# Kernel tuning notes

Hardware: AMD Instinct MI355X
Metric: run time of the kernel (lower is better)

## Reference

```python
import jax, jax.numpy as jnp
import numpy as np

B, T, D, H = 2, 2048, 1024, 16
DH = D // H  # head_dim = 64
ROPE_BASE = 10000.0


def _rope_cos_sin(seq_len, dh, dtype):
    inv_freq = 1.0 / (ROPE_BASE ** (jnp.arange(0, dh, 2, dtype=jnp.float32) / dh))
    t = jnp.arange(seq_len, dtype=jnp.float32)
    freqs = jnp.outer(t, inv_freq)            # [T, dh/2]
    emb = jnp.concatenate([freqs, freqs], -1)  # [T, dh]
    return jnp.cos(emb).astype(dtype), jnp.sin(emb).astype(dtype)


def _rotate_half(x):
    half = x.shape[-1] // 2
    return jnp.concatenate([-x[..., half:], x[..., :half]], axis=-1)


def setup_inputs() -> dict:
    key = jax.random.key(0)
    k1, k2, k3 = jax.random.split(key, 3)
    x = jax.random.normal(k1, (B, T, D), dtype=jnp.float32)
    w_qkv = jax.random.normal(k2, (D, 3 * D), dtype=jnp.float32) * (D ** -0.5)
    w_out = jax.random.normal(k3, (D, D), dtype=jnp.float32) * (D ** -0.5)
    return {"x": x, "w_qkv": w_qkv, "w_out": w_out}


def reference(x, w_qkv, w_out):
    b, t, _ = x.shape
    qkv = x @ w_qkv                                        # [B,T,3D]
    qkv = qkv.reshape(b, t, 3, H, DH).transpose(2, 0, 3, 1, 4)  # [3,B,H,T,DH]
    q, k, v = qkv[0], qkv[1], qkv[2]

    cos, sin = _rope_cos_sin(t, DH, x.dtype)               # [T,DH] each
    q = q * cos + _rotate_half(q) * sin
    k = k * cos + _rotate_half(k) * sin

    scale = DH ** -0.5
    scores = jnp.einsum('bhtd,bhsd->bhts', q, k) * scale   # [B,H,T,T]
    # dense additive causal mask (as in original module)
    neg = jnp.finfo(x.dtype).min
    causal = jnp.triu(jnp.ones((t, t), dtype=bool), k=1)
    scores = scores + jnp.where(causal, neg, jnp.zeros((), x.dtype))
    attn = jax.nn.softmax(scores, axis=-1)
    out = jnp.einsum('bhts,bhsd->bhtd', attn, v)           # [B,H,T,DH]
    out = out.transpose(0, 2, 1, 3).reshape(b, t, D)       # [B,T,D]
    return out @ w_out
```

## Files before the change

### kernel.cpp

```cpp
#include <hip/hip_runtime.h>

typedef __bf16 bf16x8 __attribute__((ext_vector_type(8)));
typedef float f32x4 __attribute__((ext_vector_type(4)));
typedef unsigned int u32x4 __attribute__((ext_vector_type(4)));
typedef unsigned int u32x2 __attribute__((ext_vector_type(2)));
typedef unsigned short u16;
typedef unsigned int u32;

#define BSZ 2
#define TSEQ 2048
#define DMODEL 1024
#define NHEAD 16
#define DHEAD 64

#define GLDS(gp, lp)                                                        \
  __builtin_amdgcn_global_load_lds(                                         \
      (const __attribute__((address_space(1))) void*)(gp),                  \
      (__attribute__((address_space(3))) void*)(lp), 16, 0, 0)

#define TRR(dst, base, OFF)                                                 \
  asm volatile("ds_read_b64_tr_b16 %0, %1 offset:" OFF                     \
               : "=v"(dst) : "v"(base) : "memory")

__device__ __forceinline__ u16 f2bf(float f) {
  return __builtin_bit_cast(u16, (__bf16)f);
}
__device__ __forceinline__ float bf2f(u16 h) {
  return __builtin_bit_cast(float, (u32)h << 16);
}

__global__ void k_cvt(const float* __restrict__ in, u16* __restrict__ out, int n4) {
  int i = blockIdx.x * 256 + threadIdx.x;
  if (i >= n4) return;
  float4 v = ((const float4*)in)[i];
  ushort4 o;
  o.x = f2bf(v.x); o.y = f2bf(v.y); o.z = f2bf(v.z); o.w = f2bf(v.w);
  ((ushort4*)out)[i] = o;
}

__global__ void k_transpose_cvt(const float* __restrict__ in, u16* __restrict__ out,
                                int K, int N) {
  __shared__ float tile[64][65];
  int n0 = blockIdx.x * 64, k0 = blockIdx.y * 64;
  int tx = threadIdx.x & 63, ty = threadIdx.x >> 6;
#pragma unroll
  for (int i = ty; i < 64; i += 4)
    tile[i][tx] = in[(size_t)(k0 + i) * N + n0 + tx];
  __syncthreads();
#pragma unroll
  for (int i = ty; i < 64; i += 4)
    out[(size_t)(n0 + i) * K + k0 + tx] = f2bf(tile[tx][i]);
}

__global__ void k_rope_table(float* __restrict__ cosT, float* __restrict__ sinT) {
  int idx = blockIdx.x * 256 + threadIdx.x;
  int t = idx >> 5, f = idx & 31;
  float inv_freq = powf(10000.0f, -(float)(2 * f) / 64.0f);
  float ang = (float)t * inv_freq;
  float s, c;
  sincosf(ang, &s, &c);
  cosT[idx] = c;
  sinT[idx] = s;
}

template <typename OutT>
__global__ __launch_bounds__(256) void k_gemm(const u16* __restrict__ A,
                                              const u16* __restrict__ Bt,
                                              OutT* __restrict__ C, int M, int N, int K) {
  __shared__ __align__(16) u16 a_lds[2][128][32];
  __shared__ __align__(16) u16 b_lds[2][128][32];
  int m0 = blockIdx.y * 128, n0 = blockIdx.x * 128;
  int tid = threadIdx.x;
  int w = tid >> 6, l = tid & 63, lr = l & 15, lg = l >> 4;
  int wr = (w >> 1) * 64, wc = (w & 1) * 64;
  int grow = l >> 2;
  int gcol = (l & 3) * 8;
  f32x4 acc[4][4] = {};

  const u16* a0 = A + (size_t)(m0 + w * 16 + grow) * K + gcol;
  const u16* a1 = A + (size_t)(m0 + (w + 4) * 16 + grow) * K + gcol;
  const u16* b0 = Bt + (size_t)(n0 + w * 16 + grow) * K + gcol;
  const u16* b1 = Bt + (size_t)(n0 + (w + 4) * 16 + grow) * K + gcol;

  int NT = K >> 5;
  GLDS(a0, &a_lds[0][w * 16][0]);
  GLDS(a1, &a_lds[0][(w + 4) * 16][0]);
  GLDS(b0, &b_lds[0][w * 16][0]);
  GLDS(b1, &b_lds[0][(w + 4) * 16][0]);

  for (int t = 0; t < NT; ++t) {
    int p = t & 1;
    if (t + 1 < NT) {
      int k0 = (t + 1) << 5;
      GLDS(a0 + k0, &a_lds[p ^ 1][w * 16][0]);
      GLDS(a1 + k0, &a_lds[p ^ 1][(w + 4) * 16][0]);
      GLDS(b0 + k0, &b_lds[p ^ 1][w * 16][0]);
      GLDS(b1 + k0, &b_lds[p ^ 1][(w + 4) * 16][0]);
      asm volatile("s_waitcnt vmcnt(4)" ::: "memory");
    } else {
      asm volatile("s_waitcnt vmcnt(0)" ::: "memory");
    }
    __builtin_amdgcn_s_barrier();
    __builtin_amdgcn_sched_barrier(0);
    bf16x8 af[4], bfv[4];
#pragma unroll
    for (int mt = 0; mt < 4; ++mt)
      af[mt] = __builtin_bit_cast(bf16x8, *(const u32x4*)&a_lds[p][wr + mt * 16 + lr][lg * 8]);
#pragma unroll
    for (int nt = 0; nt < 4; ++nt)
      bfv[nt] = __builtin_bit_cast(bf16x8, *(const u32x4*)&b_lds[p][wc + nt * 16 + lr][lg * 8]);
    __builtin_amdgcn_s_setprio(1);
#pragma unroll
    for (int mt = 0; mt < 4; ++mt)
#pragma unroll
      for (int nt = 0; nt < 4; ++nt)
        acc[mt][nt] = __builtin_amdgcn_mfma_f32_16x16x32_bf16(af[mt], bfv[nt], acc[mt][nt], 0, 0, 0);
    __builtin_amdgcn_s_setprio(0);
    __builtin_amdgcn_sched_barrier(0);
    __builtin_amdgcn_s_barrier();
  }

#pragma unroll
  for (int mt = 0; mt < 4; ++mt)
#pragma unroll
    for (int nt = 0; nt < 4; ++nt)
#pragma unroll
      for (int r = 0; r < 4; ++r) {
        int row = m0 + wr + mt * 16 + lg * 4 + r;
        int col = n0 + wc + nt * 16 + lr;
        C[(size_t)row * N + col] = acc[mt][nt][r];
      }
}

__global__ __launch_bounds__(256) void k_gemm_qkv(const u16* __restrict__ A,
                                                  const u16* __restrict__ Bt,
                                                  u16* __restrict__ Qh, u16* __restrict__ Kh,
                                                  u16* __restrict__ Vh,
                                                  const float* __restrict__ cosT,
                                                  const float* __restrict__ sinT) {
  const int M = BSZ * TSEQ, N = 3 * DMODEL, K = DMODEL;
  __shared__ __align__(16) u16 a_lds[2][128][32];
  __shared__ __align__(16) u16 b_lds[2][128][32];
  int m0 = blockIdx.y * 128, n0 = blockIdx.x * 128;
  int tid = threadIdx.x;
  int w = tid >> 6, l = tid & 63, lr = l & 15, lg = l >> 4;
  int wr = (w >> 1) * 64, wc = (w & 1) * 64;
  int grow = l >> 2;
  int gcol = (l & 3) * 8;
  f32x4 acc[4][4] = {};

  const u16* a0 = A + (size_t)(m0 + w * 16 + grow) * K + gcol;
  const u16* a1 = A + (size_t)(m0 + (w + 4) * 16 + grow) * K + gcol;
  const u16* b0 = Bt + (size_t)(n0 + w * 16 + grow) * K + gcol;
  const u16* b1 = Bt + (size_t)(n0 + (w + 4) * 16 + grow) * K + gcol;

  int NT = K >> 5;
  GLDS(a0, &a_lds[0][w * 16][0]);
  GLDS(a1, &a_lds[0][(w + 4) * 16][0]);
  GLDS(b0, &b_lds[0][w * 16][0]);
  GLDS(b1, &b_lds[0][(w + 4) * 16][0]);

  for (int t = 0; t < NT; ++t) {
    int p = t & 1;
    if (t + 1 < NT) {
      int k0 = (t + 1) << 5;
      GLDS(a0 + k0, &a_lds[p ^ 1][w * 16][0]);
      GLDS(a1 + k0, &a_lds[p ^ 1][(w + 4) * 16][0]);
      GLDS(b0 + k0, &b_lds[p ^ 1][w * 16][0]);
      GLDS(b1 + k0, &b_lds[p ^ 1][(w + 4) * 16][0]);
      asm volatile("s_waitcnt vmcnt(4)" ::: "memory");
    } else {
      asm volatile("s_waitcnt vmcnt(0)" ::: "memory");
    }
    __builtin_amdgcn_s_barrier();
    __builtin_amdgcn_sched_barrier(0);
    bf16x8 af[4], bfv[4];
#pragma unroll
    for (int mt = 0; mt < 4; ++mt)
      af[mt] = __builtin_bit_cast(bf16x8, *(const u32x4*)&a_lds[p][wr + mt * 16 + lr][lg * 8]);
#pragma unroll
    for (int nt = 0; nt < 4; ++nt)
      bfv[nt] = __builtin_bit_cast(bf16x8, *(const u32x4*)&b_lds[p][wc + nt * 16 + lr][lg * 8]);
    __builtin_amdgcn_s_setprio(1);
#pragma unroll
    for (int mt = 0; mt < 4; ++mt)
#pragma unroll
      for (int nt = 0; nt < 4; ++nt)
        acc[mt][nt] = __builtin_amdgcn_mfma_f32_16x16x32_bf16(af[mt], bfv[nt], acc[mt][nt], 0, 0, 0);
    __builtin_amdgcn_s_setprio(0);
    __builtin_amdgcn_sched_barrier(0);
    __builtin_amdgcn_s_barrier();
  }

  int sec = n0 >> 10;
  int hcol = ((n0 + wc) & 1023) >> 6;
  u16* outp = (sec == 0) ? Qh : (sec == 1) ? Kh : Vh;
  float qscale = (sec == 0) ? 0.125f : 1.0f;
#pragma unroll
  for (int mt = 0; mt < 4; ++mt)
#pragma unroll
    for (int r = 0; r < 4; ++r) {
      int row = m0 + wr + mt * 16 + lg * 4 + r;
      int b = row >> 11, tt = row & 2047;
      size_t obase = ((size_t)((b * 16 + hcol) * 2048 + tt)) * 64;
      if (sec == 2) {
#pragma unroll
        for (int nt = 0; nt < 4; ++nt)
          outp[obase + nt * 16 + lr] = f2bf(acc[mt][nt][r]);
      } else {
        float c0 = cosT[tt * 32 + lr],      s0 = sinT[tt * 32 + lr];
        float c1 = cosT[tt * 32 + 16 + lr], s1 = sinT[tt * 32 + 16 + lr];
        float v0 = acc[mt][0][r], v1 = acc[mt][1][r];
        float v2 = acc[mt][2][r], v3 = acc[mt][3][r];
        outp[obase + lr]      = f2bf((v0 * c0 - v2 * s0) * qscale);
        outp[obase + 16 + lr] = f2bf((v1 * c1 - v3 * s1) * qscale);
        outp[obase + 32 + lr] = f2bf((v2 * c0 + v0 * s0) * qscale);
        outp[obase + 48 + lr] = f2bf((v3 * c1 + v1 * s1) * qscale);
      }
    }
}

__global__ __launch_bounds__(256) void k_flash(const u16* __restrict__ Qg, const u16* __restrict__ Kg,
                                               const u16* __restrict__ Vg, u16* __restrict__ O) {
  __shared__ __align__(16) u16 k_lds[2][64][72];
  __shared__ __align__(16) u16 vsub[2][4096];
  __shared__ __align__(16) u16 p_lds[4][16][68];
  int pairIdx = blockIdx.x;
  int bh = blockIdx.y;
  int b = bh >> 4, h = bh & 15;
  size_t hoff = (size_t)bh * TSEQ * DHEAD;
  int tid = threadIdx.x, w = tid >> 6, l = tid & 63, lr = l & 15, lg = l >> 4;

  int srow = tid >> 3;
  int g8 = tid & 7;
  int sc8 = g8 * 8;
  u32 vtr0 = (u32)(uintptr_t)vsub + (u32)(lg * 1024 + lr * 8);

  const u16* kbase = Kg + hoff;
  const u16* vbase = Vg + hoff;

  for (int sub = 0; sub < 2; ++sub) {
    int qb = sub == 0 ? (31 - pairIdx) : pairIdx;

    int qrow = qb * 64 + w * 16 + lr;
    const u16* qp = Qg + hoff + (size_t)qrow * 64 + lg * 8;
    bf16x8 qf0 = __builtin_bit_cast(bf16x8, *(const u32x4*)qp);
    bf16x8 qf1 = __builtin_bit_cast(bf16x8, *(const u32x4*)(qp + 32));

    f32x4 acc[4] = {};
    float mrow[4] = {-1e30f, -1e30f, -1e30f, -1e30f};
    float lrow[4] = {0.f, 0.f, 0.f, 0.f};

    u32x4 kreg[2], vreg[2];
#pragma unroll
    for (int p = 0; p < 2; ++p) {
      int r = srow + p * 32;
      kreg[p] = *(const u32x4*)(kbase + (size_t)r * 64 + sc8);
      vreg[p] = *(const u32x4*)(vbase + (size_t)r * 64 + sc8);
    }
    __syncthreads();

    for (int kv = 0; kv <= qb; ++kv) {
      int cur = kv & 1;
#pragma unroll
      for (int p = 0; p < 2; ++p) {
        int r = srow + p * 32;
        *(u32x4*)&k_lds[cur][r][sc8] = kreg[p];
        int vo = ((r >> 2) * 4 + (g8 >> 1)) * 64 + (r & 3) * 16 + (g8 & 1) * 8;
        *(u32x4*)&vsub[cur][vo] = vreg[p];
      }
      __syncthreads();
      if (kv < qb) {
#pragma unroll
        for (int p = 0; p < 2; ++p) {
          int r = (kv + 1) * 64 + srow + p * 32;
          kreg[p] = *(const u32x4*)(kbase + (size_t)r * 64 + sc8);
          vreg[p] = *(const u32x4*)(vbase + (size_t)r * 64 + sc8);
        }
      }

      f32x4 s[4];
      __builtin_amdgcn_s_setprio(1);
#pragma unroll
      for (int c = 0; c < 4; ++c) {
        const u16* kp2 = &k_lds[cur][c * 16 + lr][lg * 8];
        bf16x8 kf0 = __builtin_bit_cast(bf16x8, *(const u32x4*)kp2);
        bf16x8 kf1 = __builtin_bit_cast(bf16x8, *(const u32x4*)(kp2 + 32));
        f32x4 z = {};
        z = __builtin_amdgcn_mfma_f32_16x16x32_bf16(qf0, kf0, z, 0, 0, 0);
        s[c] = __builtin_amdgcn_mfma_f32_16x16x32_bf16(qf1, kf1, z, 0, 0, 0);
      }
      __builtin_amdgcn_s_setprio(0);
      if (kv == qb) {
#pragma unroll
        for (int c = 0; c < 4; ++c)
#pragma unroll
          for (int r = 0; r < 4; ++r)
            if (c * 16 + lr > w * 16 + lg * 4 + r) s[c][r] = -1e30f;
      }

      float rmax[4];
#pragma unroll
      for (int r = 0; r < 4; ++r)
        rmax[r] = fmaxf(fmaxf(s[0][r], s[1][r]), fmaxf(s[2][r], s[3][r]));
#pragma unroll
      for (int mset = 1; mset <= 8; mset <<= 1)
#pragma unroll
        for (int r = 0; r < 4; ++r)
          rmax[r] = fmaxf(rmax[r], __shfl_xor(rmax[r], mset, 64));
      bool need = (rmax[0] > mrow[0] + 8.0f) | (rmax[1] > mrow[1] + 8.0f) |
                  (rmax[2] > mrow[2] + 8.0f) | (rmax[3] > mrow[3] + 8.0f);
      if (__any(need)) {
        float alpha[4];
#pragma unroll
        for (int r = 0; r < 4; ++r) {
          float mn = fmaxf(mrow[r], rmax[r]);
          alpha[r] = __expf(mrow[r] - mn);
          mrow[r] = mn;
          lrow[r] *= alpha[r];
        }
#pragma unroll
        for (int n = 0; n < 4; ++n)
#pragma unroll
          for (int r = 0; r < 4; ++r)
            acc[n][r] *= alpha[r];
      }
#pragma unroll
      for (int c = 0; c < 4; ++c)
#pragma unroll
        for (int r = 0; r < 4; ++r) {
          float pe = __expf(s[c][r] - mrow[r]);
          s[c][r] = pe;
          lrow[r] += pe;
        }

#pragma unroll
      for (int c = 0; c < 4; ++c)
#pragma unroll
        for (int r = 0; r < 4; ++r)
          p_lds[w][lg * 4 + r][c * 16 + lr] = f2bf(s[c][r]);
      bf16x8 pa0 = __builtin_bit_cast(bf16x8, *(const u32x4*)&p_lds[w][lr][lg * 8]);
      bf16x8 pa1 = __builtin_bit_cast(bf16x8, *(const u32x4*)&p_lds[w][lr][lg * 8 + 32]);

      u32 vtr = vtr0 + (u32)(cur * 8192);
      {
        u32x2 t[8];
        TRR(t[0], vtr, "0");    TRR(t[1], vtr, "512");
        TRR(t[2], vtr, "4096"); TRR(t[3], vtr, "4608");
        TRR(t[4], vtr, "128");  TRR(t[5], vtr, "640");
        TRR(t[6], vtr, "4224"); TRR(t[7], vtr, "4736");
        asm volatile("s_waitcnt lgkmcnt(0)" ::: "memory");
        __builtin_amdgcn_sched_barrier(0);
        __builtin_amdgcn_s_setprio(1);
#pragma unroll
        for (int n2 = 0; n2 < 2; ++n2) {
          u32x4 vlo, vhi;
          vlo[0] = t[n2 * 4 + 0][0]; vlo[1] = t[n2 * 4 + 0][1];
          vlo[2] = t[n2 * 4 + 1][0]; vlo[3] = t[n2 * 4 + 1][1];
          vhi[0] = t[n2 * 4 + 2][0]; vhi[1] = t[n2 * 4 + 2][1];
          vhi[2] = t[n2 * 4 + 3][0]; vhi[3] = t[n2 * 4 + 3][1];
          acc[n2] = __builtin_amdgcn_mfma_f32_16x16x32_bf16(pa0, __builtin_bit_cast(bf16x8, vlo), acc[n2], 0, 0, 0);
          acc[n2] = __builtin_amdgcn_mfma_f32_16x16x32_bf16(pa1, __builtin_bit_cast(bf16x8, vhi), acc[n2], 0, 0, 0);
        }
        __builtin_amdgcn_s_setprio(0);
      }
      {
        u32x2 t[8];
        TRR(t[0], vtr, "256");  TRR(t[1], vtr, "768");
        TRR(t[2], vtr, "4352"); TRR(t[3], vtr, "4864");
        TRR(t[4], vtr, "384");  TRR(t[5], vtr, "896");
        TRR(t[6], vtr, "4480"); TRR(t[7], vtr, "4992");
        asm volatile("s_waitcnt lgkmcnt(0)" ::: "memory");
        __builtin_amdgcn_sched_barrier(0);
        __builtin_amdgcn_s_setprio(1);
#pragma unroll
        for (int n2 = 0; n2 < 2; ++n2) {
          int n = 2 + n2;
          u32x4 vlo, vhi;
          vlo[0] = t[n2 * 4 + 0][0]; vlo[1] = t[n2 * 4 + 0][1];
          vlo[2] = t[n2 * 4 + 1][0]; vlo[3] = t[n2 * 4 + 1][1];
          vhi[0] = t[n2 * 4 + 2][0]; vhi[1] = t[n2 * 4 + 2][1];
          vhi[2] = t[n2 * 4 + 3][0]; vhi[3] = t[n2 * 4 + 3][1];
          acc[n] = __builtin_amdgcn_mfma_f32_16x16x32_bf16(pa0, __builtin_bit_cast(bf16x8, vlo), acc[n], 0, 0, 0);
          acc[n] = __builtin_amdgcn_mfma_f32_16x16x32_bf16(pa1, __builtin_bit_cast(bf16x8, vhi), acc[n], 0, 0, 0);
        }
        __builtin_amdgcn_s_setprio(0);
      }
    }

#pragma unroll
    for (int mset = 1; mset <= 8; mset <<= 1)
#pragma unroll
      for (int r = 0; r < 4; ++r)
        lrow[r] += __shfl_xor(lrow[r], mset, 64);
#pragma unroll
    for (int n = 0; n < 4; ++n)
#pragma unroll
      for (int r = 0; r < 4; ++r) {
        int t = qb * 64 + w * 16 + lg * 4 + r;
        int dd = n * 16 + lr;
        float ov = acc[n][r] / lrow[r];
        O[(size_t)(b * TSEQ + t) * DMODEL + h * 64 + dd] = f2bf(ov);
      }
  }
}

extern "C" void kernel_launch(void* const* d_in, const int* in_sizes, int n_in,
                              void* d_out, int out_size, void* d_ws, size_t ws_size,
                              hipStream_t stream) {
  const float* x     = (const float*)d_in[0];
  const float* w_qkv = (const float*)d_in[1];
  const float* w_out = (const float*)d_in[2];
  float* out = (float*)d_out;

  char* ws = (char*)d_ws;
  size_t off = 0;
  auto alloc = [&](size_t bytes) {
    char* p = ws + off;
    off += (bytes + 255) & ~(size_t)255;
    return p;
  };
  const size_t MT = (size_t)BSZ * TSEQ;
  u16* xb    = (u16*)alloc(MT * DMODEL * 2);
  u16* wqkvT = (u16*)alloc((size_t)3 * DMODEL * DMODEL * 2);
  u16* woutT = (u16*)alloc((size_t)DMODEL * DMODEL * 2);
  u16* Qh    = (u16*)alloc(MT * DMODEL * 2);
  u16* Kh    = (u16*)alloc(MT * DMODEL * 2);
  u16* Vh    = (u16*)alloc(MT * DMODEL * 2);
  u16* aout  = (u16*)alloc(MT * DMODEL * 2);
  float* cosT = (float*)alloc((size_t)TSEQ * 32 * 4);
  float* sinT = (float*)alloc((size_t)TSEQ * 32 * 4);
  if (ws_size < off) return;

  k_cvt<<<(MT * DMODEL / 4 + 255) / 256, 256, 0, stream>>>(x, xb, MT * DMODEL / 4);
  k_transpose_cvt<<<dim3(48, 16), 256, 0, stream>>>(w_qkv, wqkvT, DMODEL, 3 * DMODEL);
  k_transpose_cvt<<<dim3(16, 16), 256, 0, stream>>>(w_out, woutT, DMODEL, DMODEL);
  k_rope_table<<<(TSEQ * 32) / 256, 256, 0, stream>>>(cosT, sinT);
  k_gemm_qkv<<<dim3(24, 32), 256, 0, stream>>>(xb, wqkvT, Qh, Kh, Vh, cosT, sinT);
  k_flash<<<dim3(16, BSZ * NHEAD), 256, 0, stream>>>(Qh, Kh, Vh, aout);
  k_gemm<float><<<dim3(8, 32), 256, 0, stream>>>(aout, woutT, out, (int)MT, DMODEL, DMODEL);
}
```

Before: 218.2 us.

## Fuse prep kernels, share K/V tiles across paired query blocks, shrink out-proj tile

```diff
diff --git a/kernel.cpp b/kernel.cpp
--- a/kernel.cpp
+++ b/kernel.cpp
@@ -25,48 +25,68 @@
 __device__ __forceinline__ u16 f2bf(float f) {
   return __builtin_bit_cast(u16, (__bf16)f);
 }
+__device__ __forceinline__ u32 pack2bf(float lo, float hi) {
+  return (u32)f2bf(lo) | ((u32)f2bf(hi) << 16);
+}
 __device__ __forceinline__ float bf2f(u16 h) {
   return __builtin_bit_cast(float, (u32)h << 16);
 }
 
-__global__ void k_cvt(const float* __restrict__ in, u16* __restrict__ out, int n4) {
-  int i = blockIdx.x * 256 + threadIdx.x;
-  if (i >= n4) return;
-  float4 v = ((const float4*)in)[i];
-  ushort4 o;
-  o.x = f2bf(v.x); o.y = f2bf(v.y); o.z = f2bf(v.z); o.w = f2bf(v.w);
-  ((ushort4*)out)[i] = o;
-}
-
-__global__ void k_transpose_cvt(const float* __restrict__ in, u16* __restrict__ out,
-                                int K, int N) {
+__global__ void k_prep(const float* __restrict__ x, u16* __restrict__ xb,
+                       const float* __restrict__ wqkv, u16* __restrict__ wqkvT,
+                       const float* __restrict__ wout, u16* __restrict__ woutT,
+                       float* __restrict__ cosT, float* __restrict__ sinT) {
   __shared__ float tile[64][65];
-  int n0 = blockIdx.x * 64, k0 = blockIdx.y * 64;
-  int tx = threadIdx.x & 63, ty = threadIdx.x >> 6;
-#pragma unroll
-  for (int i = ty; i < 64; i += 4)
-    tile[i][tx] = in[(size_t)(k0 + i) * N + n0 + tx];
-  __syncthreads();
-#pragma unroll
-  for (int i = ty; i < 64; i += 4)
-    out[(size_t)(n0 + i) * K + k0 + tx] = f2bf(tile[tx][i]);
-}
-
-__global__ void k_rope_table(float* __restrict__ cosT, float* __restrict__ sinT) {
-  int idx = blockIdx.x * 256 + threadIdx.x;
-  int t = idx >> 5, f = idx & 31;
-  float inv_freq = powf(10000.0f, -(float)(2 * f) / 64.0f);
-  float ang = (float)t * inv_freq;
-  float s, c;
-  sincosf(ang, &s, &c);
-  cosT[idx] = c;
-  sinT[idx] = s;
-}
-
-template <typename OutT>
-__global__ __launch_bounds__(256) void k_gemm(const u16* __restrict__ A,
-                                              const u16* __restrict__ Bt,
-                                              OutT* __restrict__ C, int M, int N, int K) {
+  int blk = blockIdx.x, tid = threadIdx.x;
+  if (blk < 2048) {
+    int i = blk * 256 + tid;
+    const float4* f4 = (const float4*)x;
+    float4 v0 = f4[i * 2], v1 = f4[i * 2 + 1];
+    u32x4 o;
+    o[0] = pack2bf(v0.x, v0.y); o[1] = pack2bf(v0.z, v0.w);
+    o[2] = pack2bf(v1.x, v1.y); o[3] = pack2bf(v1.z, v1.w);
+    ((u32x4*)xb)[i] = o;
+  } else if (blk < 2816) {
+    int idx = blk - 2048;
+    int n0 = (idx % 48) * 64, k0 = (idx / 48) * 64;
+    int tx = tid & 63, ty = tid >> 6;
+#pragma unroll
+    for (int i = ty; i < 64; i += 4)
+      tile[i][tx] = wqkv[(size_t)(k0 + i) * 3072 + n0 + tx];
+    __syncthreads();
+#pragma unroll
+    for (int i = ty; i < 64; i += 4)
+      wqkvT[(size_t)(n0 + i) * 1024 + k0 + tx] = f2bf(tile[tx][i]);
+  } else if (blk < 3072) {
+    int idx = blk - 2816;
+    int n0 = (idx % 16) * 64, k0 = (idx / 16) * 64;
+    int tx = tid & 63, ty = tid >> 6;
+#pragma unroll
+    for (int i = ty; i < 64; i += 4)
+      tile[i][tx] = wout[(size_t)(k0 + i) * 1024 + n0 + tx];
+    __syncthreads();
+#pragma unroll
+    for (int i = ty; i < 64; i += 4)
+      woutT[(size_t)(n0 + i) * 1024 + k0 + tx] = f2bf(tile[tx][i]);
+  } else {
+    int idx = (blk - 3072) * 256 + tid;
+    int t = idx >> 5, f = idx & 31;
+    float inv_freq = powf(10000.0f, -(float)(2 * f) / 64.0f);
+    float ang = (float)t * inv_freq;
+    float s, c;
+    sincosf(ang, &s, &c);
+    cosT[idx] = c;
+    sinT[idx] = s;
+  }
+}
+
+__global__ __launch_bounds__(256) void k_gemm_qkv(const u16* __restrict__ A,
+                                                  const u16* __restrict__ Bt,
+                                                  u16* __restrict__ Qh, u16* __restrict__ Kh,
+                                                  u16* __restrict__ Vh,
+                                                  const float* __restrict__ cosT,
+                                                  const float* __restrict__ sinT) {
+  const int K = DMODEL;
   __shared__ __align__(16) u16 a_lds[2][128][32];
   __shared__ __align__(16) u16 b_lds[2][128][32];
   int m0 = blockIdx.y * 128, n0 = blockIdx.x * 128;
@@ -120,78 +140,6 @@
     __builtin_amdgcn_s_barrier();
   }
 
-#pragma unroll
-  for (int mt = 0; mt < 4; ++mt)
-#pragma unroll
-    for (int nt = 0; nt < 4; ++nt)
-#pragma unroll
-      for (int r = 0; r < 4; ++r) {
-        int row = m0 + wr + mt * 16 + lg * 4 + r;
-        int col = n0 + wc + nt * 16 + lr;
-        C[(size_t)row * N + col] = acc[mt][nt][r];
-      }
-}
-
-__global__ __launch_bounds__(256) void k_gemm_qkv(const u16* __restrict__ A,
-                                                  const u16* __restrict__ Bt,
-                                                  u16* __restrict__ Qh, u16* __restrict__ Kh,
-                                                  u16* __restrict__ Vh,
-                                                  const float* __restrict__ cosT,
-                                                  const float* __restrict__ sinT) {
-  const int M = BSZ * TSEQ, N = 3 * DMODEL, K = DMODEL;
-  __shared__ __align__(16) u16 a_lds[2][128][32];
-  __shared__ __align__(16) u16 b_lds[2][128][32];
-  int m0 = blockIdx.y * 128, n0 = blockIdx.x * 128;
-  int tid = threadIdx.x;
-  int w = tid >> 6, l = tid & 63, lr = l & 15, lg = l >> 4;
-  int wr = (w >> 1) * 64, wc = (w & 1) * 64;
-  int grow = l >> 2;
-  int gcol = (l & 3) * 8;
-  f32x4 acc[4][4] = {};
-
-  const u16* a0 = A + (size_t)(m0 + w * 16 + grow) * K + gcol;
-  const u16* a1 = A + (size_t)(m0 + (w + 4) * 16 + grow) * K + gcol;
-  const u16* b0 = Bt + (size_t)(n0 + w * 16 + grow) * K + gcol;
-  const u16* b1 = Bt + (size_t)(n0 + (w + 4) * 16 + grow) * K + gcol;
-
-  int NT = K >> 5;
-  GLDS(a0, &a_lds[0][w * 16][0]);
-  GLDS(a1, &a_lds[0][(w + 4) * 16][0]);
-  GLDS(b0, &b_lds[0][w * 16][0]);
-  GLDS(b1, &b_lds[0][(w + 4) * 16][0]);
-
-  for (int t = 0; t < NT; ++t) {
-    int p = t & 1;
-    if (t + 1 < NT) {
-      int k0 = (t + 1) << 5;
-      GLDS(a0 + k0, &a_lds[p ^ 1][w * 16][0]);
-      GLDS(a1 + k0, &a_lds[p ^ 1][(w + 4) * 16][0]);
-      GLDS(b0 + k0, &b_lds[p ^ 1][w * 16][0]);
-      GLDS(b1 + k0, &b_lds[p ^ 1][(w + 4) * 16][0]);
-      asm volatile("s_waitcnt vmcnt(4)" ::: "memory");
-    } else {
-      asm volatile("s_waitcnt vmcnt(0)" ::: "memory");
-    }
-    __builtin_amdgcn_s_barrier();
-    __builtin_amdgcn_sched_barrier(0);
-    bf16x8 af[4], bfv[4];
-#pragma unroll
-    for (int mt = 0; mt < 4; ++mt)
-      af[mt] = __builtin_bit_cast(bf16x8, *(const u32x4*)&a_lds[p][wr + mt * 16 + lr][lg * 8]);
-#pragma unroll
-    for (int nt = 0; nt < 4; ++nt)
-      bfv[nt] = __builtin_bit_cast(bf16x8, *(const u32x4*)&b_lds[p][wc + nt * 16 + lr][lg * 8]);
-    __builtin_amdgcn_s_setprio(1);
-#pragma unroll
-    for (int mt = 0; mt < 4; ++mt)
-#pragma unroll
-      for (int nt = 0; nt < 4; ++nt)
-        acc[mt][nt] = __builtin_amdgcn_mfma_f32_16x16x32_bf16(af[mt], bfv[nt], acc[mt][nt], 0, 0, 0);
-    __builtin_amdgcn_s_setprio(0);
-    __builtin_amdgcn_sched_barrier(0);
-    __builtin_amdgcn_s_barrier();
-  }
-
   int sec = n0 >> 10;
   int hcol = ((n0 + wc) & 1023) >> 6;
   u16* outp = (sec == 0) ? Qh : (sec == 1) ? Kh : Vh;
@@ -220,12 +168,79 @@
     }
 }
 
+__global__ __launch_bounds__(256) void k_gemm_out(const u16* __restrict__ A,
+                                                  const u16* __restrict__ Bt,
+                                                  float* __restrict__ C) {
+  const int N = 1024, K = 1024;
+  __shared__ __align__(16) u16 a_lds[2][128][32];
+  __shared__ __align__(16) u16 b_lds[2][64][32];
+  int m0 = blockIdx.y * 128, n0 = blockIdx.x * 64;
+  int tid = threadIdx.x;
+  int w = tid >> 6, l = tid & 63, lr = l & 15, lg = l >> 4;
+  int wr = (w >> 1) * 64, wc = (w & 1) * 32;
+  int grow = l >> 2;
+  int gcol = (l & 3) * 8;
+  f32x4 acc[4][2] = {};
+
+  const u16* a0 = A + (size_t)(m0 + w * 16 + grow) * K + gcol;
+  const u16* a1 = A + (size_t)(m0 + (w + 4) * 16 + grow) * K + gcol;
+  const u16* b0 = Bt + (size_t)(n0 + w * 16 + grow) * K + gcol;
+
+  int NT = K >> 5;
+  GLDS(a0, &a_lds[0][w * 16][0]);
+  GLDS(a1, &a_lds[0][(w + 4) * 16][0]);
+  GLDS(b0, &b_lds[0][w * 16][0]);
+
+  for (int t = 0; t < NT; ++t) {
+    int p = t & 1;
+    if (t + 1 < NT) {
+      int k0 = (t + 1) << 5;
+      GLDS(a0 + k0, &a_lds[p ^ 1][w * 16][0]);
+      GLDS(a1 + k0, &a_lds[p ^ 1][(w + 4) * 16][0]);
+      GLDS(b0 + k0, &b_lds[p ^ 1][w * 16][0]);
+      asm volatile("s_waitcnt vmcnt(3)" ::: "memory");
+    } else {
+      asm volatile("s_waitcnt vmcnt(0)" ::: "memory");
+    }
+    __builtin_amdgcn_s_barrier();
+    __builtin_amdgcn_sched_barrier(0);
+    bf16x8 af[4], bfv[2];
+#pragma unroll
+    for (int mt = 0; mt < 4; ++mt)
+      af[mt] = __builtin_bit_cast(bf16x8, *(const u32x4*)&a_lds[p][wr + mt * 16 + lr][lg * 8]);
+#pragma unroll
+    for (int nt = 0; nt < 2; ++nt)
+      bfv[nt] = __builtin_bit_cast(bf16x8, *(const u32x4*)&b_lds[p][wc + nt * 16 + lr][lg * 8]);
+    __builtin_amdgcn_s_setprio(1);
+#pragma unroll
+    for (int mt = 0; mt < 4; ++mt)
+#pragma unroll
+      for (int nt = 0; nt < 2; ++nt)
+        acc[mt][nt] = __builtin_amdgcn_mfma_f32_16x16x32_bf16(af[mt], bfv[nt], acc[mt][nt], 0, 0, 0);
+    __builtin_amdgcn_s_setprio(0);
+    __builtin_amdgcn_sched_barrier(0);
+    __builtin_amdgcn_s_barrier();
+  }
+
+#pragma unroll
+  for (int mt = 0; mt < 4; ++mt)
+#pragma unroll
+    for (int nt = 0; nt < 2; ++nt)
+#pragma unroll
+      for (int r = 0; r < 4; ++r) {
+        int row = m0 + wr + mt * 16 + lg * 4 + r;
+        int col = n0 + wc + nt * 16 + lr;
+        C[(size_t)row * N + col] = acc[mt][nt][r];
+      }
+}
+
 __global__ __launch_bounds__(256) void k_flash(const u16* __restrict__ Qg, const u16* __restrict__ Kg,
                                                const u16* __restrict__ Vg, u16* __restrict__ O) {
   __shared__ __align__(16) u16 k_lds[2][64][72];
   __shared__ __align__(16) u16 vsub[2][4096];
   __shared__ __align__(16) u16 p_lds[4][16][68];
-  int pairIdx = blockIdx.x;
+  int pp = blockIdx.x;
+  int qb1 = 31 - pp, qb2 = pp;
   int bh = blockIdx.y;
   int b = bh >> 4, h = bh & 15;
   size_t hoff = (size_t)bh * TSEQ * DHEAD;
@@ -239,66 +254,70 @@
   const u16* kbase = Kg + hoff;
   const u16* vbase = Vg + hoff;
 
-  for (int sub = 0; sub < 2; ++sub) {
-    int qb = sub == 0 ? (31 - pairIdx) : pairIdx;
-
-    int qrow = qb * 64 + w * 16 + lr;
-    const u16* qp = Qg + hoff + (size_t)qrow * 64 + lg * 8;
-    bf16x8 qf0 = __builtin_bit_cast(bf16x8, *(const u32x4*)qp);
-    bf16x8 qf1 = __builtin_bit_cast(bf16x8, *(const u32x4*)(qp + 32));
-
-    f32x4 acc[4] = {};
-    float mrow[4] = {-1e30f, -1e30f, -1e30f, -1e30f};
-    float lrow[4] = {0.f, 0.f, 0.f, 0.f};
-
-    u32x4 kreg[2], vreg[2];
+  const u16* qp1 = Qg + hoff + (size_t)(qb1 * 64 + w * 16 + lr) * 64 + lg * 8;
+  const u16* qp2 = Qg + hoff + (size_t)(qb2 * 64 + w * 16 + lr) * 64 + lg * 8;
+  bf16x8 qf0 = __builtin_bit_cast(bf16x8, *(const u32x4*)qp1);
+  bf16x8 qf1 = __builtin_bit_cast(bf16x8, *(const u32x4*)(qp1 + 32));
+  bf16x8 qg0 = __builtin_bit_cast(bf16x8, *(const u32x4*)qp2);
+  bf16x8 qg1 = __builtin_bit_cast(bf16x8, *(const u32x4*)(qp2 + 32));
+
+  f32x4 acc1[4] = {}, acc2[4] = {};
+  float m1[4] = {-1e30f, -1e30f, -1e30f, -1e30f}, m2[4] = {-1e30f, -1e30f, -1e30f, -1e30f};
+  float l1[4] = {0.f, 0.f, 0.f, 0.f}, l2[4] = {0.f, 0.f, 0.f, 0.f};
+
+  u32x4 kreg[2], vreg[2];
+#pragma unroll
+  for (int p = 0; p < 2; ++p) {
+    int r = srow + p * 32;
+    kreg[p] = *(const u32x4*)(kbase + (size_t)r * 64 + sc8);
+    vreg[p] = *(const u32x4*)(vbase + (size_t)r * 64 + sc8);
+  }
+
+  for (int kv = 0; kv <= qb1; ++kv) {
+    int cur = kv & 1;
 #pragma unroll
     for (int p = 0; p < 2; ++p) {
       int r = srow + p * 32;
-      kreg[p] = *(const u32x4*)(kbase + (size_t)r * 64 + sc8);
-      vreg[p] = *(const u32x4*)(vbase + (size_t)r * 64 + sc8);
+      *(u32x4*)&k_lds[cur][r][sc8] = kreg[p];
+      int vo = ((r >> 2) * 4 + (g8 >> 1)) * 64 + (r & 3) * 16 + (g8 & 1) * 8;
+      *(u32x4*)&vsub[cur][vo] = vreg[p];
     }
     __syncthreads();
-
-    for (int kv = 0; kv <= qb; ++kv) {
-      int cur = kv & 1;
+    if (kv < qb1) {
 #pragma unroll
       for (int p = 0; p < 2; ++p) {
-        int r = srow + p * 32;
-        *(u32x4*)&k_lds[cur][r][sc8] = kreg[p];
-        int vo = ((r >> 2) * 4 + (g8 >> 1)) * 64 + (r & 3) * 16 + (g8 & 1) * 8;
-        *(u32x4*)&vsub[cur][vo] = vreg[p];
-      }
-      __syncthreads();
-      if (kv < qb) {
-#pragma unroll
-        for (int p = 0; p < 2; ++p) {
-          int r = (kv + 1) * 64 + srow + p * 32;
-          kreg[p] = *(const u32x4*)(kbase + (size_t)r * 64 + sc8);
-          vreg[p] = *(const u32x4*)(vbase + (size_t)r * 64 + sc8);
-        }
-      }
-
+        int r = (kv + 1) * 64 + srow + p * 32;
+        kreg[p] = *(const u32x4*)(kbase + (size_t)r * 64 + sc8);
+        vreg[p] = *(const u32x4*)(vbase + (size_t)r * 64 + sc8);
+      }
+    }
+    u32 vtr = vtr0 + (u32)(cur * 8192);
+
+    bf16x8 kf0[4], kf1[4];
+#pragma unroll
+    for (int c = 0; c < 4; ++c) {
+      const u16* kp2 = &k_lds[cur][c * 16 + lr][lg * 8];
+      kf0[c] = __builtin_bit_cast(bf16x8, *(const u32x4*)kp2);
+      kf1[c] = __builtin_bit_cast(bf16x8, *(const u32x4*)(kp2 + 32));
+    }
+
+    {
       f32x4 s[4];
       __builtin_amdgcn_s_setprio(1);
 #pragma unroll
       for (int c = 0; c < 4; ++c) {
-        const u16* kp2 = &k_lds[cur][c * 16 + lr][lg * 8];
-        bf16x8 kf0 = __builtin_bit_cast(bf16x8, *(const u32x4*)kp2);
-        bf16x8 kf1 = __builtin_bit_cast(bf16x8, *(const u32x4*)(kp2 + 32));
         f32x4 z = {};
-        z = __builtin_amdgcn_mfma_f32_16x16x32_bf16(qf0, kf0, z, 0, 0, 0);
-        s[c] = __builtin_amdgcn_mfma_f32_16x16x32_bf16(qf1, kf1, z, 0, 0, 0);
+        z = __builtin_amdgcn_mfma_f32_16x16x32_bf16(qf0, kf0[c], z, 0, 0, 0);
+        s[c] = __builtin_amdgcn_mfma_f32_16x16x32_bf16(qf1, kf1[c], z, 0, 0, 0);
       }
       __builtin_amdgcn_s_setprio(0);
-      if (kv == qb) {
+      if (kv == qb1) {
 #pragma unroll
         for (int c = 0; c < 4; ++c)
 #pragma unroll
           for (int r = 0; r < 4; ++r)
             if (c * 16 + lr > w * 16 + lg * 4 + r) s[c][r] = -1e30f;
       }
-
       float rmax[4];
 #pragma unroll
       for (int r = 0; r < 4; ++r)
@@ -308,32 +327,31 @@
 #pragma unroll
         for (int r = 0; r < 4; ++r)
           rmax[r] = fmaxf(rmax[r], __shfl_xor(rmax[r], mset, 64));
-      bool need = (rmax[0] > mrow[0] + 8.0f) | (rmax[1] > mrow[1] + 8.0f) |
-                  (rmax[2] > mrow[2] + 8.0f) | (rmax[3] > mrow[3] + 8.0f);
+      bool need = (rmax[0] > m1[0] + 8.0f) | (rmax[1] > m1[1] + 8.0f) |
+                  (rmax[2] > m1[2] + 8.0f) | (rmax[3] > m1[3] + 8.0f);
       if (__any(need)) {
         float alpha[4];
 #pragma unroll
         for (int r = 0; r < 4; ++r) {
-          float mn = fmaxf(mrow[r], rmax[r]);
-          alpha[r] = __expf(mrow[r] - mn);
-          mrow[r] = mn;
-          lrow[r] *= alpha[r];
+          float mn = fmaxf(m1[r], rmax[r]);
+          alpha[r] = __expf(m1[r] - mn);
+          m1[r] = mn;
+          l1[r] *= alpha[r];
         }
 #pragma unroll
         for (int n = 0; n < 4; ++n)
 #pragma unroll
           for (int r = 0; r < 4; ++r)
-            acc[n][r] *= alpha[r];
+            acc1[n][r] *= alpha[r];
       }
 #pragma unroll
       for (int c = 0; c < 4; ++c)
 #pragma unroll
         for (int r = 0; r < 4; ++r) {
-          float pe = __expf(s[c][r] - mrow[r]);
+          float pe = __expf(s[c][r] - m1[r]);
           s[c][r] = pe;
-          lrow[r] += pe;
-        }
-
+          l1[r] += pe;
+        }
 #pragma unroll
       for (int c = 0; c < 4; ++c)
 #pragma unroll
@@ -341,8 +359,6 @@
           p_lds[w][lg * 4 + r][c * 16 + lr] = f2bf(s[c][r]);
       bf16x8 pa0 = __builtin_bit_cast(bf16x8, *(const u32x4*)&p_lds[w][lr][lg * 8]);
       bf16x8 pa1 = __builtin_bit_cast(bf16x8, *(const u32x4*)&p_lds[w][lr][lg * 8 + 32]);
-
-      u32 vtr = vtr0 + (u32)(cur * 8192);
       {
         u32x2 t[8];
         TRR(t[0], vtr, "0");    TRR(t[1], vtr, "512");
@@ -359,8 +375,8 @@
           vlo[2] = t[n2 * 4 + 1][0]; vlo[3] = t[n2 * 4 + 1][1];
           vhi[0] = t[n2 * 4 + 2][0]; vhi[1] = t[n2 * 4 + 2][1];
           vhi[2] = t[n2 * 4 + 3][0]; vhi[3] = t[n2 * 4 + 3][1];
-          acc[n2] = __builtin_amdgcn_mfma_f32_16x16x32_bf16(pa0, __builtin_bit_cast(bf16x8, vlo), acc[n2], 0, 0, 0);
-          acc[n2] = __builtin_amdgcn_mfma_f32_16x16x32_bf16(pa1, __builtin_bit_cast(bf16x8, vhi), acc[n2], 0, 0, 0);
+          acc1[n2] = __builtin_amdgcn_mfma_f32_16x16x32_bf16(pa0, __builtin_bit_cast(bf16x8, vlo), acc1[n2], 0, 0, 0);
+          acc1[n2] = __builtin_amdgcn_mfma_f32_16x16x32_bf16(pa1, __builtin_bit_cast(bf16x8, vhi), acc1[n2], 0, 0, 0);
         }
         __builtin_amdgcn_s_setprio(0);
       }
@@ -381,28 +397,134 @@
           vlo[2] = t[n2 * 4 + 1][0]; vlo[3] = t[n2 * 4 + 1][1];
           vhi[0] = t[n2 * 4 + 2][0]; vhi[1] = t[n2 * 4 + 2][1];
           vhi[2] = t[n2 * 4 + 3][0]; vhi[3] = t[n2 * 4 + 3][1];
-          acc[n] = __builtin_amdgcn_mfma_f32_16x16x32_bf16(pa0, __builtin_bit_cast(bf16x8, vlo), acc[n], 0, 0, 0);
-          acc[n] = __builtin_amdgcn_mfma_f32_16x16x32_bf16(pa1, __builtin_bit_cast(bf16x8, vhi), acc[n], 0, 0, 0);
+          acc1[n] = __builtin_amdgcn_mfma_f32_16x16x32_bf16(pa0, __builtin_bit_cast(bf16x8, vlo), acc1[n], 0, 0, 0);
+          acc1[n] = __builtin_amdgcn_mfma_f32_16x16x32_bf16(pa1, __builtin_bit_cast(bf16x8, vhi), acc1[n], 0, 0, 0);
         }
         __builtin_amdgcn_s_setprio(0);
       }
     }
 
-#pragma unroll
-    for (int mset = 1; mset <= 8; mset <<= 1)
+    if (kv <= qb2) {
+      f32x4 s[4];
+      __builtin_amdgcn_s_setprio(1);
+#pragma unroll
+      for (int c = 0; c < 4; ++c) {
+        f32x4 z = {};
+        z = __builtin_amdgcn_mfma_f32_16x16x32_bf16(qg0, kf0[c], z, 0, 0, 0);
+        s[c] = __builtin_amdgcn_mfma_f32_16x16x32_bf16(qg1, kf1[c], z, 0, 0, 0);
+      }
+      __builtin_amdgcn_s_setprio(0);
+      if (kv == qb2) {
+#pragma unroll
+        for (int c = 0; c < 4; ++c)
+#pragma unroll
+          for (int r = 0; r < 4; ++r)
+            if (c * 16 + lr > w * 16 + lg * 4 + r) s[c][r] = -1e30f;
+      }
+      float rmax[4];
 #pragma unroll
       for (int r = 0; r < 4; ++r)
-        lrow[r] += __shfl_xor(lrow[r], mset, 64);
-#pragma unroll
-    for (int n = 0; n < 4; ++n)
-#pragma unroll
-      for (int r = 0; r < 4; ++r) {
-        int t = qb * 64 + w * 16 + lg * 4 + r;
-        int dd = n * 16 + lr;
-        float ov = acc[n][r] / lrow[r];
-        O[(size_t)(b * TSEQ + t) * DMODEL + h * 64 + dd] = f2bf(ov);
-      }
+        rmax[r] = fmaxf(fmaxf(s[0][r], s[1][r]), fmaxf(s[2][r], s[3][r]));
+#pragma unroll
+      for (int mset = 1; mset <= 8; mset <<= 1)
+#pragma unroll
+        for (int r = 0; r < 4; ++r)
+          rmax[r] = fmaxf(rmax[r], __shfl_xor(rmax[r], mset, 64));
+      bool need = (rmax[0] > m2[0] + 8.0f) | (rmax[1] > m2[1] + 8.0f) |
+                  (rmax[2] > m2[2] + 8.0f) | (rmax[3] > m2[3] + 8.0f);
+      if (__any(need)) {
+        float alpha[4];
+#pragma unroll
+        for (int r = 0; r < 4; ++r) {
+          float mn = fmaxf(m2[r], rmax[r]);
+          alpha[r] = __expf(m2[r] - mn);
+          m2[r] = mn;
+          l2[r] *= alpha[r];
+        }
+#pragma unroll
+        for (int n = 0; n < 4; ++n)
+#pragma unroll
+          for (int r = 0; r < 4; ++r)
+            acc2[n][r] *= alpha[r];
+      }
+#pragma unroll
+      for (int c = 0; c < 4; ++c)
+#pragma unroll
+        for (int r = 0; r < 4; ++r) {
+          float pe = __expf(s[c][r] - m2[r]);
+          s[c][r] = pe;
+          l2[r] += pe;
+        }
+#pragma unroll
+      for (int c = 0; c < 4; ++c)
+#pragma unroll
+        for (int r = 0; r < 4; ++r)
+          p_lds[w][lg * 4 + r][c * 16 + lr] = f2bf(s[c][r]);
+      bf16x8 pa0 = __builtin_bit_cast(bf16x8, *(const u32x4*)&p_lds[w][lr][lg * 8]);
+      bf16x8 pa1 = __builtin_bit_cast(bf16x8, *(const u32x4*)&p_lds[w][lr][lg * 8 + 32]);
+      {
+        u32x2 t[8];
+        TRR(t[0], vtr, "0");    TRR(t[1], vtr, "512");
+        TRR(t[2], vtr, "4096"); TRR(t[3], vtr, "4608");
+        TRR(t[4], vtr, "128");  TRR(t[5], vtr, "640");
+        TRR(t[6], vtr, "4224"); TRR(t[7], vtr, "4736");
+        asm volatile("s_waitcnt lgkmcnt(0)" ::: "memory");
+        __builtin_amdgcn_sched_barrier(0);
+        __builtin_amdgcn_s_setprio(1);
+#pragma unroll
+        for (int n2 = 0; n2 < 2; ++n2) {
+          u32x4 vlo, vhi;
+          vlo[0] = t[n2 * 4 + 0][0]; vlo[1] = t[n2 * 4 + 0][1];
+          vlo[2] = t[n2 * 4 + 1][0]; vlo[3] = t[n2 * 4 + 1][1];
+          vhi[0] = t[n2 * 4 + 2][0]; vhi[1] = t[n2 * 4 + 2][1];
+          vhi[2] = t[n2 * 4 + 3][0]; vhi[3] = t[n2 * 4 + 3][1];
+          acc2[n2] = __builtin_amdgcn_mfma_f32_16x16x32_bf16(pa0, __builtin_bit_cast(bf16x8, vlo), acc2[n2], 0, 0, 0);
+          acc2[n2] = __builtin_amdgcn_mfma_f32_16x16x32_bf16(pa1, __builtin_bit_cast(bf16x8, vhi), acc2[n2], 0, 0, 0);
+        }
+        __builtin_amdgcn_s_setprio(0);
+      }
+      {
+        u32x2 t[8];
+        TRR(t[0], vtr, "256");  TRR(t[1], vtr, "768");
+        TRR(t[2], vtr, "4352"); TRR(t[3], vtr, "4864");
+        TRR(t[4], vtr, "384");  TRR(t[5], vtr, "896");
+        TRR(t[6], vtr, "4480"); TRR(t[7], vtr, "4992");
+        asm volatile("s_waitcnt lgkmcnt(0)" ::: "memory");
+        __builtin_amdgcn_sched_barrier(0);
+        __builtin_amdgcn_s_setprio(1);
+#pragma unroll
+        for (int n2 = 0; n2 < 2; ++n2) {
+          int n = 2 + n2;
+          u32x4 vlo, vhi;
+          vlo[0] = t[n2 * 4 + 0][0]; vlo[1] = t[n2 * 4 + 0][1];
+          vlo[2] = t[n2 * 4 + 1][0]; vlo[3] = t[n2 * 4 + 1][1];
+          vhi[0] = t[n2 * 4 + 2][0]; vhi[1] = t[n2 * 4 + 2][1];
+          vhi[2] = t[n2 * 4 + 3][0]; vhi[3] = t[n2 * 4 + 3][1];
+          acc2[n] = __builtin_amdgcn_mfma_f32_16x16x32_bf16(pa0, __builtin_bit_cast(bf16x8, vlo), acc2[n], 0, 0, 0);
+          acc2[n] = __builtin_amdgcn_mfma_f32_16x16x32_bf16(pa1, __builtin_bit_cast(bf16x8, vhi), acc2[n], 0, 0, 0);
+        }
+        __builtin_amdgcn_s_setprio(0);
+      }
+    }
   }
+
+#pragma unroll
+  for (int mset = 1; mset <= 8; mset <<= 1)
+#pragma unroll
+    for (int r = 0; r < 4; ++r) {
+      l1[r] += __shfl_xor(l1[r], mset, 64);
+      l2[r] += __shfl_xor(l2[r], mset, 64);
+    }
+#pragma unroll
+  for (int n = 0; n < 4; ++n)
+#pragma unroll
+    for (int r = 0; r < 4; ++r) {
+      int t1 = qb1 * 64 + w * 16 + lg * 4 + r;
+      int t2 = qb2 * 64 + w * 16 + lg * 4 + r;
+      int dd = n * 16 + lr;
+      O[(size_t)(b * TSEQ + t1) * DMODEL + h * 64 + dd] = f2bf(acc1[n][r] / l1[r]);
+      O[(size_t)(b * TSEQ + t2) * DMODEL + h * 64 + dd] = f2bf(acc2[n][r] / l2[r]);
+    }
 }
 
 extern "C" void kernel_launch(void* const* d_in, const int* in_sizes, int n_in,
@@ -432,11 +554,8 @@
   float* sinT = (float*)alloc((size_t)TSEQ * 32 * 4);
   if (ws_size < off) return;
 
-  k_cvt<<<(MT * DMODEL / 4 + 255) / 256, 256, 0, stream>>>(x, xb, MT * DMODEL / 4);
-  k_transpose_cvt<<<dim3(48, 16), 256, 0, stream>>>(w_qkv, wqkvT, DMODEL, 3 * DMODEL);
-  k_transpose_cvt<<<dim3(16, 16), 256, 0, stream>>>(w_out, woutT, DMODEL, DMODEL);
-  k_rope_table<<<(TSEQ * 32) / 256, 256, 0, stream>>>(cosT, sinT);
+  k_prep<<<3328, 256, 0, stream>>>(x, xb, w_qkv, wqkvT, w_out, woutT, cosT, sinT);
   k_gemm_qkv<<<dim3(24, 32), 256, 0, stream>>>(xb, wqkvT, Qh, Kh, Vh, cosT, sinT);
   k_flash<<<dim3(16, BSZ * NHEAD), 256, 0, stream>>>(Qh, Kh, Vh, aout);
-  k_gemm<float><<<dim3(8, 32), 256, 0, stream>>>(aout, woutT, out, (int)MT, DMODEL, DMODEL);
-}
+  k_gemm_out<<<dim3(16, 32), 256, 0, stream>>>(aout, woutT, out);
+}
```

Measured after the change: 202.4 us. 1.08x faster.
